# Kernel optimization log

Measured on AMD Instinct MI355X. Metric: run time of the kernel, lower is better.

The kernel has to match this reference:

```python
import jax, jax.numpy as jnp
import numpy as np

EPS_NORM = 1e-12   # F.normalize eps
EPS_PD = 1e-6      # torch pairwise_distance eps
MARGIN = 1.0       # TripletMarginLoss margin


def _l2norm(x, axis):
    n = jnp.sqrt(jnp.sum(x * x, axis=axis, keepdims=True))
    return x / jnp.maximum(n, EPS_NORM)


def setup_inputs() -> dict:
    key = jax.random.key(0)
    k1, k2 = jax.random.split(key)
    query = jax.random.normal(k1, (64, 512, 32, 32), dtype=jnp.float32)
    keys = jax.random.normal(k2, (512, 512), dtype=jnp.float32)
    return {"query": query, "keys": keys}


def reference(query, keys):
    # train=True path of Memory.forward
    B, dims, h, w = query.shape
    m, d = keys.shape
    q = _l2norm(query, axis=1)                       # normalize over channel dim
    q = jnp.transpose(q, (0, 2, 3, 1))               # [B, h, w, d]
    q_flat = q.reshape(B * h * w, d)                 # [N, d]

    score = q_flat @ keys.T                          # [N, m]
    score_query = jax.nn.softmax(score, axis=0)      # softmax over samples per slot
    score_memory = jax.nn.softmax(score, axis=1)     # softmax over slots per sample

    # --- gather loss: MSE(query, keys[argmax slot].detach()) ---
    gather_idx = jnp.argmax(score_memory, axis=1)    # [N]
    nearest = jax.lax.stop_gradient(keys[gather_idx])
    gathering_loss = jnp.mean((q_flat - nearest) ** 2)

    # --- spread loss: triplet(query, 1st-NN slot, 2nd-NN slot) ---
    _, top2 = jax.lax.top_k(score_memory, 2)         # [N, 2]
    pos = jax.lax.stop_gradient(keys[top2[:, 0]])
    neg = jax.lax.stop_gradient(keys[top2[:, 1]])
    d_pos = jnp.linalg.norm(q_flat - pos + EPS_PD, axis=1)
    d_neg = jnp.linalg.norm(q_flat - neg + EPS_PD, axis=1)
    spreading_loss = jnp.mean(jnp.maximum(d_pos - d_neg + MARGIN, 0.0))

    # --- read: attention over memory with detached softmax weights ---
    concat_memory = jax.lax.stop_gradient(score_memory) @ keys      # [N, d]
    updated_query = jnp.concatenate([q_flat, concat_memory], axis=1)
    updated_query = updated_query.reshape(B, h, w, 2 * dims)
    updated_query = jnp.transpose(updated_query, (0, 3, 1, 2))      # [B, 2d, h, w]

    # --- update: argmax-grouped weighted scatter-sum into memory slots ---
    # weight_n = score_query[n, g_n] / max_k score_query[k, g_n]
    col_max = jnp.max(score_query, axis=0)                          # [m]
    wgt = jnp.take_along_axis(score_query, gather_idx[:, None], axis=1)[:, 0]
    wgt = wgt / col_max[gather_idx]                                 # [N]
    query_update = jax.ops.segment_sum(wgt[:, None] * q_flat, gather_idx,
                                       num_segments=m)              # [m, d]
    updated_memory = _l2norm(query_update + keys, axis=1)
    updated_memory = jax.lax.stop_gradient(updated_memory)

    return (updated_query, updated_memory, score_query, score_memory,
            gathering_loss, spreading_loss)
```

## Files before the change

kernel.cpp:

```cpp
#include <hip/hip_runtime.h>
#include <stdint.h>


typedef unsigned int u32;
typedef unsigned long long u64;
typedef unsigned short u16;

typedef float f32x4 __attribute__((ext_vector_type(4)));
typedef short bf16x8 __attribute__((ext_vector_type(8)));

#define DIMS 512

__device__ __forceinline__ u16 f2bf(float x){
  u32 u = __float_as_uint(x);
  return (u16)((u + 0x7FFFu + ((u >> 16) & 1u)) >> 16);
}
__device__ __forceinline__ float bf2f(u16 h){ return __uint_as_float(((u32)h) << 16); }
__device__ __forceinline__ u32 pack2(float a, float b){
  return (u32)f2bf(a) | ((u32)f2bf(b) << 16);
}
__device__ __forceinline__ u32 fkey(float x){
  u32 b = __float_as_uint(x);
  return (b & 0x80000000u) ? ~b : (b | 0x80000000u);
}
__device__ __forceinline__ float fdec(u32 u){
  return (u & 0x80000000u) ? __uint_as_float(u & 0x7FFFFFFFu) : __uint_as_float(~u);
}
__device__ __forceinline__ void gload16(char* lds, const void* g){
  __builtin_amdgcn_global_load_lds(
      (const __attribute__((address_space(1))) u32*)g,
      (__attribute__((address_space(3))) u32*)lds, 16, 0, 0);
}

__global__ __launch_bounds__(512) void k0_prep(const float* __restrict__ keys,
    u16* __restrict__ kb, u16* __restrict__ kt,
    float* __restrict__ kn2, float* __restrict__ ksum,
    u32* __restrict__ colmax_u, float* __restrict__ colsum)
{
  const int j = blockIdx.x, t = threadIdx.x;
  float v = keys[(size_t)j * 512 + t];
  u16 h = f2bf(v);
  kb[(size_t)j * 512 + t] = h;
  kt[(size_t)t * 512 + j] = h;
  float s = v, ss = v * v;
  #pragma unroll
  for (int d = 1; d < 64; d <<= 1){ s += __shfl_xor(s, d); ss += __shfl_xor(ss, d); }
  __shared__ float rs[8], rss[8];
  const int w = t >> 6, lane = t & 63;
  if (lane == 0){ rs[w] = s; rss[w] = ss; }
  __syncthreads();
  if (t == 0){
    float S = 0.f, SS = 0.f;
    for (int i = 0; i < 8; ++i){ S += rs[i]; SS += rss[i]; }
    ksum[j] = S; kn2[j] = SS;
  }
  if (j == 0){ colmax_u[t] = 0u; colsum[t] = 0.f; }
}

__global__ __launch_bounds__(256) void k1_norm(const float* __restrict__ query,
    float* __restrict__ uq, u16* __restrict__ qb, float* __restrict__ sumq)
{
  __shared__ float red[4][64];
  __shared__ float rinvS[64];
  __shared__ float T[64][65];
  const int t = threadIdx.x;
  const int p = t & 63;
  const int cq = t >> 6;
  const int b = blockIdx.y;
  const int p0 = blockIdx.x * 64;
  const float* base = query + (size_t)b * 524288 + p0;

  float v[128];
  float ssq = 0.f;
  #pragma unroll
  for (int k = 0; k < 128; ++k){
    float x = base[(size_t)(cq + 4 * k) * 1024 + p];
    v[k] = x; ssq += x * x;
  }
  red[cq][p] = ssq;
  __syncthreads();
  if (t < 64){
    float tot = red[0][t] + red[1][t] + red[2][t] + red[3][t];
    rinvS[t] = 1.0f / fmaxf(sqrtf(tot), 1e-12f);
  }
  __syncthreads();
  const float rinv = rinvS[p];
  float* uqo = uq + (size_t)b * 1048576 + p0;
  float mysum = 0.f;
  const int r = t >> 2, seg = t & 3;
  for (int cb = 0; cb < 8; ++cb){
    #pragma unroll
    for (int i = 0; i < 16; ++i){
      int c = cb * 64 + cq + i * 4;
      float x = v[cb * 16 + i] * rinv;
      uqo[(size_t)c * 1024 + p] = x;
      T[cq + i * 4][p] = x;
      mysum += x;
    }
    __syncthreads();
    {
      u32 wpk[8];
      #pragma unroll
      for (int k = 0; k < 8; ++k)
        wpk[k] = pack2(T[seg * 16 + 2 * k][r], T[seg * 16 + 2 * k + 1][r]);
      uint4* dst = (uint4*)(qb + ((size_t)(b * 1024 + p0 + r)) * 512 + cb * 64 + seg * 16);
      dst[0] = make_uint4(wpk[0], wpk[1], wpk[2], wpk[3]);
      dst[1] = make_uint4(wpk[4], wpk[5], wpk[6], wpk[7]);
    }
    __syncthreads();
  }
  red[cq][p] = mysum;
  __syncthreads();
  if (t < 64)
    sumq[(size_t)b * 1024 + p0 + t] = red[0][t] + red[1][t] + red[2][t] + red[3][t];
}

__global__ __launch_bounds__(512) void k2f(const u16* __restrict__ Aq,
    const u16* __restrict__ Bk, float* __restrict__ SM,
    u32* __restrict__ colmax_u, float* __restrict__ colsum,
    int* __restrict__ gidx, float* __restrict__ s1v, float* __restrict__ rfac,
    const float* __restrict__ kn2, const float* __restrict__ ksum,
    const float* __restrict__ sumq, float* __restrict__ part)
{
  __shared__ __align__(16) char As[4096];
  __shared__ __align__(16) char Bs[32768];
  __shared__ float rs_m1[8][64], rs_m2[8][64], rs_es[8][64];
  __shared__ int   rs_i1[8][64], rs_i2[8][64];
  __shared__ float rtinv[64];

  const int t = threadIdx.x;
  const int w = t >> 6;
  const int lane = t & 63;
  const int l15 = lane & 15, l4 = lane >> 4;
  const int n0 = blockIdx.x * 64;

  f32x4 acc[4][4];
  #pragma unroll
  for (int a = 0; a < 4; ++a)
    #pragma unroll
    for (int b = 0; b < 4; ++b) acc[a][b] = (f32x4){0.f, 0.f, 0.f, 0.f};

  const int lrow = lane >> 2;
  const int lpos = lane & 3;
  const u16* srcB[4];
  #pragma unroll
  for (int i = 0; i < 4; ++i){
    int r = w * 64 + i * 16 + lrow;
    srcB[i] = Bk + (size_t)r * 512 + ((lpos ^ ((r >> 1) & 3)) * 8);
  }
  const u16* srcA = Aq;
  {
    int r = (w & 3) * 16 + lrow;
    srcA = Aq + (size_t)(n0 + r) * 512 + ((lpos ^ ((r >> 1) & 3)) * 8);
  }
  char* ldsB = Bs + w * 4096;
  char* ldsA = As + (w & 3) * 1024;

  for (int kk = 0; kk < 16; ++kk){
    const int ko = kk * 32;
    __syncthreads();
    #pragma unroll
    for (int i = 0; i < 4; ++i)
      gload16(ldsB + i * 1024, srcB[i] + ko);
    if (w < 4) gload16(ldsA, srcA + ko);
    __syncthreads();
    bf16x8 af[4], bf[4];
    #pragma unroll
    for (int mi = 0; mi < 4; ++mi){
      int rr = mi * 16 + l15;
      af[mi] = *(const bf16x8*)(As + rr * 64 + ((l4 ^ ((rr >> 1) & 3)) * 16));
    }
    #pragma unroll
    for (int nj = 0; nj < 4; ++nj){
      int rb = w * 64 + nj * 16 + l15;
      bf[nj] = *(const bf16x8*)(Bs + rb * 64 + ((l4 ^ ((rb >> 1) & 3)) * 16));
    }
    #pragma unroll
    for (int mi = 0; mi < 4; ++mi)
      #pragma unroll
      for (int nj = 0; nj < 4; ++nj)
        acc[mi][nj] = __builtin_amdgcn_mfma_f32_16x16x32_bf16(af[mi], bf[nj], acc[mi][nj], 0, 0, 0);
  }

  #pragma unroll
  for (int mi = 0; mi < 4; ++mi){
    #pragma unroll
    for (int e = 0; e < 4; ++e){
      const int row = mi * 16 + l4 * 4 + e;
      float m1 = -3e38f, m2 = -3e38f; int i1 = 0x7FFFFFFF, i2 = 0x7FFFFFFF;
      #pragma unroll
      for (int nj = 0; nj < 4; ++nj){
        float val = acc[mi][nj][e];
        int idx = w * 64 + nj * 16 + l15;
        if (val > m1){ m2 = m1; i2 = i1; m1 = val; i1 = idx; }
        else if (val > m2){ m2 = val; i2 = idx; }
      }
      #pragma unroll
      for (int d = 1; d < 16; d <<= 1){
        float o1 = __shfl_xor(m1, d), o2 = __shfl_xor(m2, d);
        int oi1 = __shfl_xor(i1, d), oi2 = __shfl_xor(i2, d);
        if (o1 > m1 || (o1 == m1 && oi1 < i1)){
          if (m1 > o2 || (m1 == o2 && i1 < oi2)){ m2 = m1; i2 = i1; }
          else { m2 = o2; i2 = oi2; }
          m1 = o1; i1 = oi1;
        } else {
          if (o1 > m2 || (o1 == m2 && oi1 < i2)){ m2 = o1; i2 = oi1; }
        }
      }
      if (l15 == 0){
        rs_m1[w][row] = m1; rs_i1[w][row] = i1;
        rs_m2[w][row] = m2; rs_i2[w][row] = i2;
      }
    }
  }
  #pragma unroll
  for (int nj = 0; nj < 4; ++nj){
    float cm = -3e38f;
    #pragma unroll
    for (int mi = 0; mi < 4; ++mi)
      #pragma unroll
      for (int e = 0; e < 4; ++e) cm = fmaxf(cm, acc[mi][nj][e]);
    cm = fmaxf(cm, __shfl_xor(cm, 16));
    cm = fmaxf(cm, __shfl_xor(cm, 32));
    if (l4 == 0) atomicMax(&colmax_u[w * 64 + nj * 16 + l15], fkey(cm));
  }
  #pragma unroll
  for (int mi = 0; mi < 4; ++mi)
    #pragma unroll
    for (int nj = 0; nj < 4; ++nj)
      #pragma unroll
      for (int e = 0; e < 4; ++e) acc[mi][nj][e] = expf(acc[mi][nj][e]);
  #pragma unroll
  for (int mi = 0; mi < 4; ++mi){
    #pragma unroll
    for (int e = 0; e < 4; ++e){
      const int row = mi * 16 + l4 * 4 + e;
      float ps = acc[mi][0][e] + acc[mi][1][e] + acc[mi][2][e] + acc[mi][3][e];
      #pragma unroll
      for (int d = 1; d < 16; d <<= 1) ps += __shfl_xor(ps, d);
      if (l15 == 0) rs_es[w][row] = ps;
    }
  }
  #pragma unroll
  for (int nj = 0; nj < 4; ++nj){
    float cs = 0.f;
    #pragma unroll
    for (int mi = 0; mi < 4; ++mi)
      #pragma unroll
      for (int e = 0; e < 4; ++e) cs += acc[mi][nj][e];
    cs += __shfl_xor(cs, 16);
    cs += __shfl_xor(cs, 32);
    if (l4 == 0) atomicAdd(&colsum[w * 64 + nj * 16 + l15], cs);
  }
  __syncthreads();
  if (t < 64){
    const int row = t, n = n0 + row;
    float m1 = -3e38f, m2 = -3e38f; int i1 = 0x7FFFFFFF, i2 = 0x7FFFFFFF;
    float tot = 0.f;
    #pragma unroll
    for (int w2 = 0; w2 < 8; ++w2){
      float o1 = rs_m1[w2][row], o2 = rs_m2[w2][row];
      int oi1 = rs_i1[w2][row], oi2 = rs_i2[w2][row];
      tot += rs_es[w2][row];
      if (o1 > m1 || (o1 == m1 && oi1 < i1)){
        if (m1 > o2 || (m1 == o2 && i1 < oi2)){ m2 = m1; i2 = i1; }
        else { m2 = o2; i2 = oi2; }
        m1 = o1; i1 = oi1;
      } else {
        if (o1 > m2 || (o1 == m2 && oi1 < i2)){ m2 = o1; i2 = oi1; }
      }
    }
    gidx[n] = i1; s1v[n] = m1; rfac[n] = tot;
    rtinv[row] = 1.0f / tot;
    float sq = sumq[n];
    float gl = 1.0f + kn2[i1] - 2.0f * m1;
    float dp2 = gl + 2e-6f * (sq - ksum[i1]) + 5.12e-10f;
    float dn2 = 1.0f + kn2[i2] - 2.0f * m2 + 2e-6f * (sq - ksum[i2]) + 5.12e-10f;
    float sl = fmaxf(sqrtf(dp2) - sqrtf(dn2) + 1.0f, 0.0f);
    #pragma unroll
    for (int d = 1; d < 64; d <<= 1){ gl += __shfl_xor(gl, d); sl += __shfl_xor(sl, d); }
    if (t == 0){ part[2 * blockIdx.x] = gl; part[2 * blockIdx.x + 1] = sl; }
  }
  __syncthreads();
  #pragma unroll
  for (int mi = 0; mi < 4; ++mi){
    #pragma unroll
    for (int e = 0; e < 4; ++e){
      const int row = mi * 16 + l4 * 4 + e;
      const float ri = rtinv[row];
      float* dst = SM + (size_t)(n0 + row) * 512 + w * 64 + l15;
      #pragma unroll
      for (int nj = 0; nj < 4; ++nj)
        dst[nj * 16] = acc[mi][nj][e] * ri;
    }
  }
}

__global__ __launch_bounds__(256) void k7_update(const int* __restrict__ gidx,
    const float* __restrict__ s1v, const u32* __restrict__ colmax_u,
    const u16* __restrict__ qb, const float* __restrict__ keys, float* __restrict__ um)
{
  const int j = blockIdx.x;
  const int t = threadIdx.x;
  const int lane = t & 63;
  const int w = t >> 6;
  const float cm = fdec(colmax_u[j]);
  float acc[8] = {0.f, 0.f, 0.f, 0.f, 0.f, 0.f, 0.f, 0.f};
  const int b0 = w * 16384, b1 = b0 + 16384;
  for (int base = b0; base < b1; base += 64){
    u64 mask = __ballot(gidx[base + lane] == j);
    while (mask){
      int bpos = (int)__builtin_ctzll(mask);
      mask &= mask - 1;
      int rrow = base + bpos;
      float wgt = expf(s1v[rrow] - cm);
      uint4 rv = *(const uint4*)(qb + (size_t)rrow * 512 + lane * 8);
      u32 a4[4] = {rv.x, rv.y, rv.z, rv.w};
      #pragma unroll
      for (int q = 0; q < 4; ++q){
        acc[2 * q]     += wgt * bf2f((u16)(a4[q] & 0xFFFFu));
        acc[2 * q + 1] += wgt * bf2f((u16)(a4[q] >> 16));
      }
    }
  }
  __shared__ float red[512];
  for (int i = t; i < 512; i += 256) red[i] = 0.f;
  __syncthreads();
  #pragma unroll
  for (int k = 0; k < 8; ++k) atomicAdd(&red[lane * 8 + k], acc[k]);
  __syncthreads();
  float v0 = red[t]       + keys[(size_t)j * 512 + t];
  float v1 = red[t + 256] + keys[(size_t)j * 512 + t + 256];
  float ssq = v0 * v0 + v1 * v1;
  #pragma unroll
  for (int d = 1; d < 64; d <<= 1) ssq += __shfl_xor(ssq, d);
  __shared__ float rr4[4];
  if (lane == 0) rr4[w] = ssq;
  __syncthreads();
  const float rinv = 1.0f / fmaxf(sqrtf(rr4[0] + rr4[1] + rr4[2] + rr4[3]), 1e-12f);
  um[(size_t)j * 512 + t]       = v0 * rinv;
  um[(size_t)j * 512 + t + 256] = v1 * rinv;
}

__global__ __launch_bounds__(512) void k6f(const float* __restrict__ SMf,
    const u16* __restrict__ kt, float* __restrict__ Uq, float* __restrict__ SQ,
    const float* __restrict__ rfac, const float* __restrict__ colsum)
{
  __shared__ __align__(16) char Ks[32768];
  __shared__ __align__(16) char Qs[4096];
  const int t = threadIdx.x;
  const int w = t >> 6;
  const int lane = t & 63;
  const int l15 = lane & 15, l4 = lane >> 4;
  const int n0 = blockIdx.x * 64;

  f32x4 acc[4][4];
  #pragma unroll
  for (int a = 0; a < 4; ++a)
    #pragma unroll
    for (int b = 0; b < 4; ++b) acc[a][b] = (f32x4){0.f, 0.f, 0.f, 0.f};

  const int lrow = lane >> 2;
  const int lpos = lane & 3;
  const u16* srcK[4];
  #pragma unroll
  for (int i = 0; i < 4; ++i){
    int r = w * 64 + i * 16 + lrow;
    srcK[i] = kt + (size_t)r * 512 + ((lpos ^ ((r >> 1) & 3)) * 8);
  }
  char* ldsK = Ks + w * 4096;
  const int rQ = t >> 3;
  const int c4 = (t & 7) * 4;
  const size_t qrow = (size_t)(n0 + rQ) * 512;
  const float rf = rfac[n0 + rQ];
  const int qdst = rQ * 64 + (((c4 >> 3) ^ ((rQ >> 1) & 3)) * 16) + ((c4 & 4) << 1);

  float4 q0 = *(const float4*)(SMf + qrow + c4);

  for (int kk = 0; kk < 16; ++kk){
    const int ko = kk * 32;
    __syncthreads();
    *(u32*)(Qs + qdst)     = pack2(q0.x, q0.y);
    *(u32*)(Qs + qdst + 4) = pack2(q0.z, q0.w);
    #pragma unroll
    for (int i = 0; i < 4; ++i)
      gload16(ldsK + i * 1024, srcK[i] + ko);
    {
      float4 cs = *(const float4*)(colsum + ko + c4);
      float4 sq;
      sq.x = q0.x * rf / cs.x; sq.y = q0.y * rf / cs.y;
      sq.z = q0.z * rf / cs.z; sq.w = q0.w * rf / cs.w;
      *(float4*)(SQ + qrow + ko + c4) = sq;
    }
    __syncthreads();
    if (kk < 15) q0 = *(const float4*)(SMf + qrow + ko + 32 + c4);
    bf16x8 af[4], bf[4];
    #pragma unroll
    for (int mi = 0; mi < 4; ++mi){
      int rr = w * 64 + mi * 16 + l15;
      af[mi] = *(const bf16x8*)(Ks + rr * 64 + ((l4 ^ ((rr >> 1) & 3)) * 16));
    }
    #pragma unroll
    for (int nj = 0; nj < 4; ++nj){
      int rb = nj * 16 + l15;
      bf[nj] = *(const bf16x8*)(Qs + rb * 64 + ((l4 ^ ((rb >> 1) & 3)) * 16));
    }
    #pragma unroll
    for (int mi = 0; mi < 4; ++mi)
      #pragma unroll
      for (int nj = 0; nj < 4; ++nj)
        acc[mi][nj] = __builtin_amdgcn_mfma_f32_16x16x32_bf16(af[mi], bf[nj], acc[mi][nj], 0, 0, 0);
  }

  const int bq = n0 >> 10;
  const int p0 = n0 & 1023;
  #pragma unroll
  for (int mi = 0; mi < 4; ++mi){
    #pragma unroll
    for (int e = 0; e < 4; ++e){
      const int chn = w * 64 + mi * 16 + l4 * 4 + e;
      float* dst = Uq + (size_t)(bq * 1024 + 512 + chn) * 1024 + p0 + l15;
      #pragma unroll
      for (int nj = 0; nj < 4; ++nj)
        dst[nj * 16] = acc[mi][nj][e];
    }
  }
}

__global__ __launch_bounds__(256) void k9_fin(const float* __restrict__ part,
    float* __restrict__ outL)
{
  const int t = threadIdx.x;
  float gs = 0.f, ss = 0.f;
  for (int i = t; i < 1024; i += 256){ gs += part[2 * i]; ss += part[2 * i + 1]; }
  #pragma unroll
  for (int d = 1; d < 64; d <<= 1){ gs += __shfl_xor(gs, d); ss += __shfl_xor(ss, d); }
  __shared__ float rg[4], rs2[4];
  if ((t & 63) == 0){ rg[t >> 6] = gs; rs2[t >> 6] = ss; }
  __syncthreads();
  if (t == 0){
    float G = rg[0] + rg[1] + rg[2] + rg[3];
    float S = rs2[0] + rs2[1] + rs2[2] + rs2[3];
    outL[0] = G / (65536.0f * 512.0f);
    outL[1] = S / 65536.0f;
  }
}

extern "C" void kernel_launch(void* const* d_in, const int* in_sizes, int n_in,
                              void* d_out, int out_size, void* d_ws, size_t ws_size,
                              hipStream_t stream)
{
  int qi = 0, ki = 1;
  if (n_in >= 2 && in_sizes[0] < in_sizes[1]){ qi = 1; ki = 0; }
  const float* query = (const float*)d_in[qi];
  const float* keys  = (const float*)d_in[ki];
  float* out = (float*)d_out;

  const size_t OFF_UQ = 0;
  const size_t OFF_UM = 67108864;
  const size_t OFF_SQ = 67371008;
  const size_t OFF_SM = 100925440;
  const size_t OFF_GL = 134479872;

  u16* qb = (u16*)(out + OFF_SQ);

  char* ws = (char*)d_ws;
  u16*   kb     = (u16*)ws;
  u16*   kt     = (u16*)(ws + 524288);
  float* sumq   = (float*)(ws + 1048576);
  int*   gidx   = (int*)(ws + 1310720);
  float* s1v    = (float*)(ws + 1572864);
  float* rfac   = (float*)(ws + 1835008);
  float* part   = (float*)(ws + 2097152);
  float* kn2    = (float*)(ws + 2105344);
  float* ksum   = (float*)(ws + 2107392);
  u32*   colmax = (u32*)(ws + 2109440);
  float* colsum = (float*)(ws + 2111488);

  k0_prep<<<512, 512, 0, stream>>>(keys, kb, kt, kn2, ksum, colmax, colsum);
  k1_norm<<<dim3(16, 64), 256, 0, stream>>>(query, out + OFF_UQ, qb, sumq);
  k2f<<<1024, 512, 0, stream>>>(qb, kb, out + OFF_SM, colmax, colsum,
                                gidx, s1v, rfac, kn2, ksum, sumq, part);
  k7_update<<<512, 256, 0, stream>>>(gidx, s1v, colmax, qb, keys, out + OFF_UM);
  k6f<<<1024, 512, 0, stream>>>(out + OFF_SM, kt, out + OFF_UQ, out + OFF_SQ,
                                rfac, colsum);
  k9_fin<<<1, 256, 0, stream>>>(part, out + OFF_GL);
}
```

Baseline: 384.5 us.

## Double-buffer LDS tiles in k2f and k6f GEMMs; widen k7_update to 512 threads

The GEMM loops in k2f and k6f now ping-pong between two LDS buffers. Each iteration issues the next k-slice's global-to-LDS loads before running the MFMAs on the current slice, which removes one barrier per iteration and hides load latency. Separately, k7_update runs with 512 threads, so each wave scans half as many samples. The LDS footprint grows to 72KB per block, which may lower occupancy, and the reduction scratch arrays now alias the B buffer region after the loop.

```diff
diff --git a/kernel.cpp b/kernel.cpp
--- a/kernel.cpp
+++ b/kernel.cpp
@@ -122,12 +122,7 @@
     const float* __restrict__ kn2, const float* __restrict__ ksum,
     const float* __restrict__ sumq, float* __restrict__ part)
 {
-  __shared__ __align__(16) char As[4096];
-  __shared__ __align__(16) char Bs[32768];
-  __shared__ float rs_m1[8][64], rs_m2[8][64], rs_es[8][64];
-  __shared__ int   rs_i1[8][64], rs_i2[8][64];
-  __shared__ float rtinv[64];
-
+  __shared__ __align__(16) char smem[73728];
   const int t = threadIdx.x;
   const int w = t >> 6;
   const int lane = t & 63;
@@ -148,22 +143,32 @@
     int r = w * 64 + i * 16 + lrow;
     srcB[i] = Bk + (size_t)r * 512 + ((lpos ^ ((r >> 1) & 3)) * 8);
   }
-  const u16* srcA = Aq;
+  const u16* srcA;
   {
     int r = (w & 3) * 16 + lrow;
     srcA = Aq + (size_t)(n0 + r) * 512 + ((lpos ^ ((r >> 1) & 3)) * 8);
   }
-  char* ldsB = Bs + w * 4096;
-  char* ldsA = As + (w & 3) * 1024;
+
+  {
+    char* ldsB = smem + 8192 + w * 4096;
+    #pragma unroll
+    for (int i = 0; i < 4; ++i) gload16(ldsB + i * 1024, srcB[i]);
+    if (w < 4) gload16(smem + (w & 3) * 1024, srcA);
+  }
+  __syncthreads();
 
   for (int kk = 0; kk < 16; ++kk){
-    const int ko = kk * 32;
-    __syncthreads();
-    #pragma unroll
-    for (int i = 0; i < 4; ++i)
-      gload16(ldsB + i * 1024, srcB[i] + ko);
-    if (w < 4) gload16(ldsA, srcA + ko);
-    __syncthreads();
+    const int cur = kk & 1;
+    if (kk < 15){
+      const int nxt = cur ^ 1;
+      const int ko = (kk + 1) * 32;
+      char* ldsB = smem + 8192 + nxt * 32768 + w * 4096;
+      #pragma unroll
+      for (int i = 0; i < 4; ++i) gload16(ldsB + i * 1024, srcB[i] + ko);
+      if (w < 4) gload16(smem + nxt * 4096 + (w & 3) * 1024, srcA + ko);
+    }
+    const char* As = smem + cur * 4096;
+    const char* Bs = smem + 8192 + cur * 32768;
     bf16x8 af[4], bf[4];
     #pragma unroll
     for (int mi = 0; mi < 4; ++mi){
@@ -180,7 +185,15 @@
       #pragma unroll
       for (int nj = 0; nj < 4; ++nj)
         acc[mi][nj] = __builtin_amdgcn_mfma_f32_16x16x32_bf16(af[mi], bf[nj], acc[mi][nj], 0, 0, 0);
-  }
+    __syncthreads();
+  }
+
+  float* rs_m1 = (float*)(smem + 8192);
+  float* rs_m2 = (float*)(smem + 10240);
+  float* rs_es = (float*)(smem + 12288);
+  int*   rs_i1 = (int*)(smem + 14336);
+  int*   rs_i2 = (int*)(smem + 16384);
+  float* rtinv = (float*)(smem + 18432);
 
   #pragma unroll
   for (int mi = 0; mi < 4; ++mi){
@@ -208,8 +221,8 @@
         }
       }
       if (l15 == 0){
-        rs_m1[w][row] = m1; rs_i1[w][row] = i1;
-        rs_m2[w][row] = m2; rs_i2[w][row] = i2;
+        rs_m1[w * 64 + row] = m1; rs_i1[w * 64 + row] = i1;
+        rs_m2[w * 64 + row] = m2; rs_i2[w * 64 + row] = i2;
       }
     }
   }
@@ -238,7 +251,7 @@
       float ps = acc[mi][0][e] + acc[mi][1][e] + acc[mi][2][e] + acc[mi][3][e];
       #pragma unroll
       for (int d = 1; d < 16; d <<= 1) ps += __shfl_xor(ps, d);
-      if (l15 == 0) rs_es[w][row] = ps;
+      if (l15 == 0) rs_es[w * 64 + row] = ps;
     }
   }
   #pragma unroll
@@ -259,9 +272,9 @@
     float tot = 0.f;
     #pragma unroll
     for (int w2 = 0; w2 < 8; ++w2){
-      float o1 = rs_m1[w2][row], o2 = rs_m2[w2][row];
-      int oi1 = rs_i1[w2][row], oi2 = rs_i2[w2][row];
-      tot += rs_es[w2][row];
+      float o1 = rs_m1[w2 * 64 + row], o2 = rs_m2[w2 * 64 + row];
+      int oi1 = rs_i1[w2 * 64 + row], oi2 = rs_i2[w2 * 64 + row];
+      tot += rs_es[w2 * 64 + row];
       if (o1 > m1 || (o1 == m1 && oi1 < i1)){
         if (m1 > o2 || (m1 == o2 && i1 < oi2)){ m2 = m1; i2 = i1; }
         else { m2 = o2; i2 = oi2; }
@@ -296,7 +309,7 @@
   }
 }
 
-__global__ __launch_bounds__(256) void k7_update(const int* __restrict__ gidx,
+__global__ __launch_bounds__(512) void k7_update(const int* __restrict__ gidx,
     const float* __restrict__ s1v, const u32* __restrict__ colmax_u,
     const u16* __restrict__ qb, const float* __restrict__ keys, float* __restrict__ um)
 {
@@ -306,7 +319,7 @@
   const int w = t >> 6;
   const float cm = fdec(colmax_u[j]);
   float acc[8] = {0.f, 0.f, 0.f, 0.f, 0.f, 0.f, 0.f, 0.f};
-  const int b0 = w * 16384, b1 = b0 + 16384;
+  const int b0 = w * 8192, b1 = b0 + 8192;
   for (int base = b0; base < b1; base += 64){
     u64 mask = __ballot(gidx[base + lane] == j);
     while (mask){
@@ -324,30 +337,28 @@
     }
   }
   __shared__ float red[512];
-  for (int i = t; i < 512; i += 256) red[i] = 0.f;
+  red[t] = 0.f;
   __syncthreads();
   #pragma unroll
   for (int k = 0; k < 8; ++k) atomicAdd(&red[lane * 8 + k], acc[k]);
   __syncthreads();
-  float v0 = red[t]       + keys[(size_t)j * 512 + t];
-  float v1 = red[t + 256] + keys[(size_t)j * 512 + t + 256];
-  float ssq = v0 * v0 + v1 * v1;
+  float v0 = red[t] + keys[(size_t)j * 512 + t];
+  float ssq = v0 * v0;
   #pragma unroll
   for (int d = 1; d < 64; d <<= 1) ssq += __shfl_xor(ssq, d);
-  __shared__ float rr4[4];
-  if (lane == 0) rr4[w] = ssq;
-  __syncthreads();
-  const float rinv = 1.0f / fmaxf(sqrtf(rr4[0] + rr4[1] + rr4[2] + rr4[3]), 1e-12f);
-  um[(size_t)j * 512 + t]       = v0 * rinv;
-  um[(size_t)j * 512 + t + 256] = v1 * rinv;
+  __shared__ float rr8[8];
+  if (lane == 0) rr8[w] = ssq;
+  __syncthreads();
+  float tot = rr8[0] + rr8[1] + rr8[2] + rr8[3] + rr8[4] + rr8[5] + rr8[6] + rr8[7];
+  const float rinv = 1.0f / fmaxf(sqrtf(tot), 1e-12f);
+  um[(size_t)j * 512 + t] = v0 * rinv;
 }
 
 __global__ __launch_bounds__(512) void k6f(const float* __restrict__ SMf,
     const u16* __restrict__ kt, float* __restrict__ Uq, float* __restrict__ SQ,
     const float* __restrict__ rfac, const float* __restrict__ colsum)
 {
-  __shared__ __align__(16) char Ks[32768];
-  __shared__ __align__(16) char Qs[4096];
+  __shared__ __align__(16) char smem[73728];
   const int t = threadIdx.x;
   const int w = t >> 6;
   const int lane = t & 63;
@@ -368,32 +379,49 @@
     int r = w * 64 + i * 16 + lrow;
     srcK[i] = kt + (size_t)r * 512 + ((lpos ^ ((r >> 1) & 3)) * 8);
   }
-  char* ldsK = Ks + w * 4096;
   const int rQ = t >> 3;
   const int c4 = (t & 7) * 4;
   const size_t qrow = (size_t)(n0 + rQ) * 512;
   const float rf = rfac[n0 + rQ];
   const int qdst = rQ * 64 + (((c4 >> 3) ^ ((rQ >> 1) & 3)) * 16) + ((c4 & 4) << 1);
 
-  float4 q0 = *(const float4*)(SMf + qrow + c4);
+  float4 qcur = *(const float4*)(SMf + qrow + c4);
+  {
+    char* Qs0 = smem + 65536;
+    *(u32*)(Qs0 + qdst)     = pack2(qcur.x, qcur.y);
+    *(u32*)(Qs0 + qdst + 4) = pack2(qcur.z, qcur.w);
+    float4 cs = *(const float4*)(colsum + c4);
+    float4 sq;
+    sq.x = qcur.x * rf / cs.x; sq.y = qcur.y * rf / cs.y;
+    sq.z = qcur.z * rf / cs.z; sq.w = qcur.w * rf / cs.w;
+    *(float4*)(SQ + qrow + c4) = sq;
+    char* ldsK = smem + w * 4096;
+    #pragma unroll
+    for (int i = 0; i < 4; ++i) gload16(ldsK + i * 1024, srcK[i]);
+  }
+  float4 qnext = *(const float4*)(SMf + qrow + 32 + c4);
+  __syncthreads();
 
   for (int kk = 0; kk < 16; ++kk){
-    const int ko = kk * 32;
-    __syncthreads();
-    *(u32*)(Qs + qdst)     = pack2(q0.x, q0.y);
-    *(u32*)(Qs + qdst + 4) = pack2(q0.z, q0.w);
-    #pragma unroll
-    for (int i = 0; i < 4; ++i)
-      gload16(ldsK + i * 1024, srcK[i] + ko);
-    {
+    const int cur = kk & 1;
+    if (kk < 15){
+      const int nxt = cur ^ 1;
+      const int ko = (kk + 1) * 32;
+      char* ldsK = smem + nxt * 32768 + w * 4096;
+      #pragma unroll
+      for (int i = 0; i < 4; ++i) gload16(ldsK + i * 1024, srcK[i] + ko);
+      char* QsN = smem + 65536 + nxt * 4096;
+      *(u32*)(QsN + qdst)     = pack2(qnext.x, qnext.y);
+      *(u32*)(QsN + qdst + 4) = pack2(qnext.z, qnext.w);
       float4 cs = *(const float4*)(colsum + ko + c4);
       float4 sq;
-      sq.x = q0.x * rf / cs.x; sq.y = q0.y * rf / cs.y;
-      sq.z = q0.z * rf / cs.z; sq.w = q0.w * rf / cs.w;
+      sq.x = qnext.x * rf / cs.x; sq.y = qnext.y * rf / cs.y;
+      sq.z = qnext.z * rf / cs.z; sq.w = qnext.w * rf / cs.w;
       *(float4*)(SQ + qrow + ko + c4) = sq;
-    }
-    __syncthreads();
-    if (kk < 15) q0 = *(const float4*)(SMf + qrow + ko + 32 + c4);
+      if (kk < 14) qnext = *(const float4*)(SMf + qrow + ko + 32 + c4);
+    }
+    const char* Ks = smem + cur * 32768;
+    const char* Qs = smem + 65536 + cur * 4096;
     bf16x8 af[4], bf[4];
     #pragma unroll
     for (int mi = 0; mi < 4; ++mi){
@@ -410,6 +438,7 @@
       #pragma unroll
       for (int nj = 0; nj < 4; ++nj)
         acc[mi][nj] = __builtin_amdgcn_mfma_f32_16x16x32_bf16(af[mi], bf[nj], acc[mi][nj], 0, 0, 0);
+    __syncthreads();
   }
 
   const int bq = n0 >> 10;
@@ -481,7 +510,7 @@
   k1_norm<<<dim3(16, 64), 256, 0, stream>>>(query, out + OFF_UQ, qb, sumq);
   k2f<<<1024, 512, 0, stream>>>(qb, kb, out + OFF_SM, colmax, colsum,
                                 gidx, s1v, rfac, kn2, ksum, sumq, part);
-  k7_update<<<512, 256, 0, stream>>>(gidx, s1v, colmax, qb, keys, out + OFF_UM);
+  k7_update<<<512, 512, 0, stream>>>(gidx, s1v, colmax, qb, keys, out + OFF_UM);
   k6f<<<1024, 512, 0, stream>>>(out + OFF_SM, kt, out + OFF_UQ, out + OFF_SQ,
                                 rfac, colsum);
   k9_fin<<<1, 256, 0, stream>>>(part, out + OFF_GL);
```

Measured after the change: 375.0 us (median of 2 runs). 1.03x faster.

## Replace LDS staging in GEMM kernels with direct register double-buffered loads

Applied to the files above, without the earlier changes.

Both MFMA GEMM kernels (k2f score and k6f read) drop their LDS tiles, barriers and global_load_lds staging. Each wave now loads its bf16x8 fragments straight from global memory into registers, double-buffered across k-steps, and raises wave priority around the MFMA bursts. In k6f the fp32 softmax rows are converted to bf16 in registers, and wave 0 alone writes score_query using precomputed reciprocals. k7_update moves to 512 threads per block so each wave scans half as many rows. The trade is that every wave re-fetches shared A/B data from global or L2 memory instead of sharing one LDS copy, in exchange for removing the syncthreads stalls, and register pressure goes up.

```diff
diff --git a/kernel.cpp b/kernel.cpp
--- a/kernel.cpp
+++ b/kernel.cpp
@@ -25,11 +25,6 @@
 }
 __device__ __forceinline__ float fdec(u32 u){
   return (u & 0x80000000u) ? __uint_as_float(u & 0x7FFFFFFFu) : __uint_as_float(~u);
-}
-__device__ __forceinline__ void gload16(char* lds, const void* g){
-  __builtin_amdgcn_global_load_lds(
-      (const __attribute__((address_space(1))) u32*)g,
-      (__attribute__((address_space(3))) u32*)lds, 16, 0, 0);
 }
 
 __global__ __launch_bounds__(512) void k0_prep(const float* __restrict__ keys,
@@ -122,8 +117,6 @@
     const float* __restrict__ kn2, const float* __restrict__ ksum,
     const float* __restrict__ sumq, float* __restrict__ part)
 {
-  __shared__ __align__(16) char As[4096];
-  __shared__ __align__(16) char Bs[32768];
   __shared__ float rs_m1[8][64], rs_m2[8][64], rs_es[8][64];
   __shared__ int   rs_i1[8][64], rs_i2[8][64];
   __shared__ float rtinv[64];
@@ -140,46 +133,48 @@
     #pragma unroll
     for (int b = 0; b < 4; ++b) acc[a][b] = (f32x4){0.f, 0.f, 0.f, 0.f};
 
-  const int lrow = lane >> 2;
-  const int lpos = lane & 3;
-  const u16* srcB[4];
-  #pragma unroll
-  for (int i = 0; i < 4; ++i){
-    int r = w * 64 + i * 16 + lrow;
-    srcB[i] = Bk + (size_t)r * 512 + ((lpos ^ ((r >> 1) & 3)) * 8);
-  }
-  const u16* srcA = Aq;
-  {
-    int r = (w & 3) * 16 + lrow;
-    srcA = Aq + (size_t)(n0 + r) * 512 + ((lpos ^ ((r >> 1) & 3)) * 8);
-  }
-  char* ldsB = Bs + w * 4096;
-  char* ldsA = As + (w & 3) * 1024;
-
-  for (int kk = 0; kk < 16; ++kk){
-    const int ko = kk * 32;
-    __syncthreads();
-    #pragma unroll
-    for (int i = 0; i < 4; ++i)
-      gload16(ldsB + i * 1024, srcB[i] + ko);
-    if (w < 4) gload16(ldsA, srcA + ko);
-    __syncthreads();
-    bf16x8 af[4], bf[4];
-    #pragma unroll
-    for (int mi = 0; mi < 4; ++mi){
-      int rr = mi * 16 + l15;
-      af[mi] = *(const bf16x8*)(As + rr * 64 + ((l4 ^ ((rr >> 1) & 3)) * 16));
-    }
-    #pragma unroll
-    for (int nj = 0; nj < 4; ++nj){
-      int rb = w * 64 + nj * 16 + l15;
-      bf[nj] = *(const bf16x8*)(Bs + rb * 64 + ((l4 ^ ((rb >> 1) & 3)) * 16));
-    }
+  const u16* ap[4];
+  const u16* bp[4];
+  #pragma unroll
+  for (int mi = 0; mi < 4; ++mi)
+    ap[mi] = Aq + (size_t)(n0 + mi * 16 + l15) * 512 + l4 * 8;
+  #pragma unroll
+  for (int nj = 0; nj < 4; ++nj)
+    bp[nj] = Bk + (size_t)(w * 64 + nj * 16 + l15) * 512 + l4 * 8;
+
+  bf16x8 a0[4], b0[4], a1[4], b1[4];
+  #pragma unroll
+  for (int mi = 0; mi < 4; ++mi) a0[mi] = *(const bf16x8*)(ap[mi]);
+  #pragma unroll
+  for (int nj = 0; nj < 4; ++nj) b0[nj] = *(const bf16x8*)(bp[nj]);
+
+  for (int kk = 0; kk < 16; kk += 2){
+    const int ko1 = (kk + 1) * 32;
+    #pragma unroll
+    for (int mi = 0; mi < 4; ++mi) a1[mi] = *(const bf16x8*)(ap[mi] + ko1);
+    #pragma unroll
+    for (int nj = 0; nj < 4; ++nj) b1[nj] = *(const bf16x8*)(bp[nj] + ko1);
+    __builtin_amdgcn_s_setprio(1);
     #pragma unroll
     for (int mi = 0; mi < 4; ++mi)
       #pragma unroll
       for (int nj = 0; nj < 4; ++nj)
-        acc[mi][nj] = __builtin_amdgcn_mfma_f32_16x16x32_bf16(af[mi], bf[nj], acc[mi][nj], 0, 0, 0);
+        acc[mi][nj] = __builtin_amdgcn_mfma_f32_16x16x32_bf16(a0[mi], b0[nj], acc[mi][nj], 0, 0, 0);
+    __builtin_amdgcn_s_setprio(0);
+    if (kk + 2 < 16){
+      const int ko2 = (kk + 2) * 32;
+      #pragma unroll
+      for (int mi = 0; mi < 4; ++mi) a0[mi] = *(const bf16x8*)(ap[mi] + ko2);
+      #pragma unroll
+      for (int nj = 0; nj < 4; ++nj) b0[nj] = *(const bf16x8*)(bp[nj] + ko2);
+    }
+    __builtin_amdgcn_s_setprio(1);
+    #pragma unroll
+    for (int mi = 0; mi < 4; ++mi)
+      #pragma unroll
+      for (int nj = 0; nj < 4; ++nj)
+        acc[mi][nj] = __builtin_amdgcn_mfma_f32_16x16x32_bf16(a1[mi], b1[nj], acc[mi][nj], 0, 0, 0);
+    __builtin_amdgcn_s_setprio(0);
   }
 
   #pragma unroll
@@ -296,7 +291,7 @@
   }
 }
 
-__global__ __launch_bounds__(256) void k7_update(const int* __restrict__ gidx,
+__global__ __launch_bounds__(512) void k7_update(const int* __restrict__ gidx,
     const float* __restrict__ s1v, const u32* __restrict__ colmax_u,
     const u16* __restrict__ qb, const float* __restrict__ keys, float* __restrict__ um)
 {
@@ -306,7 +301,7 @@
   const int w = t >> 6;
   const float cm = fdec(colmax_u[j]);
   float acc[8] = {0.f, 0.f, 0.f, 0.f, 0.f, 0.f, 0.f, 0.f};
-  const int b0 = w * 16384, b1 = b0 + 16384;
+  const int b0 = w * 8192, b1 = b0 + 8192;
   for (int base = b0; base < b1; base += 64){
     u64 mask = __ballot(gidx[base + lane] == j);
     while (mask){
@@ -324,30 +319,27 @@
     }
   }
   __shared__ float red[512];
-  for (int i = t; i < 512; i += 256) red[i] = 0.f;
+  red[t] = 0.f;
   __syncthreads();
   #pragma unroll
   for (int k = 0; k < 8; ++k) atomicAdd(&red[lane * 8 + k], acc[k]);
   __syncthreads();
-  float v0 = red[t]       + keys[(size_t)j * 512 + t];
-  float v1 = red[t + 256] + keys[(size_t)j * 512 + t + 256];
-  float ssq = v0 * v0 + v1 * v1;
+  float v0 = red[t] + keys[(size_t)j * 512 + t];
+  float ssq = v0 * v0;
   #pragma unroll
   for (int d = 1; d < 64; d <<= 1) ssq += __shfl_xor(ssq, d);
-  __shared__ float rr4[4];
-  if (lane == 0) rr4[w] = ssq;
-  __syncthreads();
-  const float rinv = 1.0f / fmaxf(sqrtf(rr4[0] + rr4[1] + rr4[2] + rr4[3]), 1e-12f);
-  um[(size_t)j * 512 + t]       = v0 * rinv;
-  um[(size_t)j * 512 + t + 256] = v1 * rinv;
+  __shared__ float rr8[8];
+  if (lane == 0) rr8[w] = ssq;
+  __syncthreads();
+  float tot = rr8[0] + rr8[1] + rr8[2] + rr8[3] + rr8[4] + rr8[5] + rr8[6] + rr8[7];
+  const float rinv = 1.0f / fmaxf(sqrtf(tot), 1e-12f);
+  um[(size_t)j * 512 + t] = v0 * rinv;
 }
 
 __global__ __launch_bounds__(512) void k6f(const float* __restrict__ SMf,
     const u16* __restrict__ kt, float* __restrict__ Uq, float* __restrict__ SQ,
     const float* __restrict__ rfac, const float* __restrict__ colsum)
 {
-  __shared__ __align__(16) char Ks[32768];
-  __shared__ __align__(16) char Qs[4096];
   const int t = threadIdx.x;
   const int w = t >> 6;
   const int lane = t & 63;
@@ -360,56 +352,122 @@
     #pragma unroll
     for (int b = 0; b < 4; ++b) acc[a][b] = (f32x4){0.f, 0.f, 0.f, 0.f};
 
-  const int lrow = lane >> 2;
-  const int lpos = lane & 3;
-  const u16* srcK[4];
-  #pragma unroll
-  for (int i = 0; i < 4; ++i){
-    int r = w * 64 + i * 16 + lrow;
-    srcK[i] = kt + (size_t)r * 512 + ((lpos ^ ((r >> 1) & 3)) * 8);
-  }
-  char* ldsK = Ks + w * 4096;
-  const int rQ = t >> 3;
-  const int c4 = (t & 7) * 4;
-  const size_t qrow = (size_t)(n0 + rQ) * 512;
-  const float rf = rfac[n0 + rQ];
-  const int qdst = rQ * 64 + (((c4 >> 3) ^ ((rQ >> 1) & 3)) * 16) + ((c4 & 4) << 1);
-
-  float4 q0 = *(const float4*)(SMf + qrow + c4);
-
-  for (int kk = 0; kk < 16; ++kk){
-    const int ko = kk * 32;
-    __syncthreads();
-    *(u32*)(Qs + qdst)     = pack2(q0.x, q0.y);
-    *(u32*)(Qs + qdst + 4) = pack2(q0.z, q0.w);
-    #pragma unroll
-    for (int i = 0; i < 4; ++i)
-      gload16(ldsK + i * 1024, srcK[i] + ko);
+  const u16* ap[4];
+  const float* bpf[4];
+  #pragma unroll
+  for (int mi = 0; mi < 4; ++mi)
+    ap[mi] = kt + (size_t)(w * 64 + mi * 16 + l15) * 512 + l4 * 8;
+  #pragma unroll
+  for (int nj = 0; nj < 4; ++nj)
+    bpf[nj] = SMf + (size_t)(n0 + nj * 16 + l15) * 512 + l4 * 8;
+
+  float rf4[4];
+  #pragma unroll
+  for (int nj = 0; nj < 4; ++nj) rf4[nj] = rfac[n0 + nj * 16 + l15];
+
+  bf16x8 a0[4], a1[4];
+  float4 pA[4][2], pB[4][2];
+  #pragma unroll
+  for (int mi = 0; mi < 4; ++mi) a0[mi] = *(const bf16x8*)(ap[mi]);
+  #pragma unroll
+  for (int nj = 0; nj < 4; ++nj){
+    pA[nj][0] = *(const float4*)(bpf[nj]);
+    pA[nj][1] = *(const float4*)(bpf[nj] + 4);
+  }
+
+  for (int kk = 0; kk < 16; kk += 2){
+    const int ko1 = (kk + 1) * 32;
+    #pragma unroll
+    for (int mi = 0; mi < 4; ++mi) a1[mi] = *(const bf16x8*)(ap[mi] + ko1);
+    #pragma unroll
+    for (int nj = 0; nj < 4; ++nj){
+      pB[nj][0] = *(const float4*)(bpf[nj] + ko1);
+      pB[nj][1] = *(const float4*)(bpf[nj] + ko1 + 4);
+    }
     {
-      float4 cs = *(const float4*)(colsum + ko + c4);
-      float4 sq;
-      sq.x = q0.x * rf / cs.x; sq.y = q0.y * rf / cs.y;
-      sq.z = q0.z * rf / cs.z; sq.w = q0.w * rf / cs.w;
-      *(float4*)(SQ + qrow + ko + c4) = sq;
-    }
-    __syncthreads();
-    if (kk < 15) q0 = *(const float4*)(SMf + qrow + ko + 32 + c4);
-    bf16x8 af[4], bf[4];
-    #pragma unroll
-    for (int mi = 0; mi < 4; ++mi){
-      int rr = w * 64 + mi * 16 + l15;
-      af[mi] = *(const bf16x8*)(Ks + rr * 64 + ((l4 ^ ((rr >> 1) & 3)) * 16));
-    }
-    #pragma unroll
-    for (int nj = 0; nj < 4; ++nj){
-      int rb = nj * 16 + l15;
-      bf[nj] = *(const bf16x8*)(Qs + rb * 64 + ((l4 ^ ((rb >> 1) & 3)) * 16));
-    }
-    #pragma unroll
-    for (int mi = 0; mi < 4; ++mi)
-      #pragma unroll
-      for (int nj = 0; nj < 4; ++nj)
-        acc[mi][nj] = __builtin_amdgcn_mfma_f32_16x16x32_bf16(af[mi], bf[nj], acc[mi][nj], 0, 0, 0);
+      bf16x8 bb[4];
+      u32* bw;
+      #pragma unroll
+      for (int nj = 0; nj < 4; ++nj){
+        u32 w0 = pack2(pA[nj][0].x, pA[nj][0].y);
+        u32 w1 = pack2(pA[nj][0].z, pA[nj][0].w);
+        u32 w2 = pack2(pA[nj][1].x, pA[nj][1].y);
+        u32 w3 = pack2(pA[nj][1].z, pA[nj][1].w);
+        bw = (u32*)&bb[nj];
+        bw[0] = w0; bw[1] = w1; bw[2] = w2; bw[3] = w3;
+      }
+      if (w == 0){
+        const int cbase = kk * 32 + l4 * 8;
+        float4 cs0 = *(const float4*)(colsum + cbase);
+        float4 cs1 = *(const float4*)(colsum + cbase + 4);
+        float4 ci0 = {1.f / cs0.x, 1.f / cs0.y, 1.f / cs0.z, 1.f / cs0.w};
+        float4 ci1 = {1.f / cs1.x, 1.f / cs1.y, 1.f / cs1.z, 1.f / cs1.w};
+        #pragma unroll
+        for (int nj = 0; nj < 4; ++nj){
+          float* d = SQ + (size_t)(n0 + nj * 16 + l15) * 512 + cbase;
+          float4 s0 = {pA[nj][0].x * rf4[nj] * ci0.x, pA[nj][0].y * rf4[nj] * ci0.y,
+                       pA[nj][0].z * rf4[nj] * ci0.z, pA[nj][0].w * rf4[nj] * ci0.w};
+          float4 s1 = {pA[nj][1].x * rf4[nj] * ci1.x, pA[nj][1].y * rf4[nj] * ci1.y,
+                       pA[nj][1].z * rf4[nj] * ci1.z, pA[nj][1].w * rf4[nj] * ci1.w};
+          *(float4*)(d) = s0;
+          *(float4*)(d + 4) = s1;
+        }
+      }
+      __builtin_amdgcn_s_setprio(1);
+      #pragma unroll
+      for (int mi = 0; mi < 4; ++mi)
+        #pragma unroll
+        for (int nj = 0; nj < 4; ++nj)
+          acc[mi][nj] = __builtin_amdgcn_mfma_f32_16x16x32_bf16(a0[mi], bb[nj], acc[mi][nj], 0, 0, 0);
+      __builtin_amdgcn_s_setprio(0);
+    }
+    if (kk + 2 < 16){
+      const int ko2 = (kk + 2) * 32;
+      #pragma unroll
+      for (int mi = 0; mi < 4; ++mi) a0[mi] = *(const bf16x8*)(ap[mi] + ko2);
+      #pragma unroll
+      for (int nj = 0; nj < 4; ++nj){
+        pA[nj][0] = *(const float4*)(bpf[nj] + ko2);
+        pA[nj][1] = *(const float4*)(bpf[nj] + ko2 + 4);
+      }
+    }
+    {
+      bf16x8 bb[4];
+      u32* bw;
+      #pragma unroll
+      for (int nj = 0; nj < 4; ++nj){
+        u32 w0 = pack2(pB[nj][0].x, pB[nj][0].y);
+        u32 w1 = pack2(pB[nj][0].z, pB[nj][0].w);
+        u32 w2 = pack2(pB[nj][1].x, pB[nj][1].y);
+        u32 w3 = pack2(pB[nj][1].z, pB[nj][1].w);
+        bw = (u32*)&bb[nj];
+        bw[0] = w0; bw[1] = w1; bw[2] = w2; bw[3] = w3;
+      }
+      if (w == 0){
+        const int cbase = (kk + 1) * 32 + l4 * 8;
+        float4 cs0 = *(const float4*)(colsum + cbase);
+        float4 cs1 = *(const float4*)(colsum + cbase + 4);
+        float4 ci0 = {1.f / cs0.x, 1.f / cs0.y, 1.f / cs0.z, 1.f / cs0.w};
+        float4 ci1 = {1.f / cs1.x, 1.f / cs1.y, 1.f / cs1.z, 1.f / cs1.w};
+        #pragma unroll
+        for (int nj = 0; nj < 4; ++nj){
+          float* d = SQ + (size_t)(n0 + nj * 16 + l15) * 512 + cbase;
+          float4 s0 = {pB[nj][0].x * rf4[nj] * ci0.x, pB[nj][0].y * rf4[nj] * ci0.y,
+                       pB[nj][0].z * rf4[nj] * ci0.z, pB[nj][0].w * rf4[nj] * ci0.w};
+          float4 s1 = {pB[nj][1].x * rf4[nj] * ci1.x, pB[nj][1].y * rf4[nj] * ci1.y,
+                       pB[nj][1].z * rf4[nj] * ci1.z, pB[nj][1].w * rf4[nj] * ci1.w};
+          *(float4*)(d) = s0;
+          *(float4*)(d + 4) = s1;
+        }
+      }
+      __builtin_amdgcn_s_setprio(1);
+      #pragma unroll
+      for (int mi = 0; mi < 4; ++mi)
+        #pragma unroll
+        for (int nj = 0; nj < 4; ++nj)
+          acc[mi][nj] = __builtin_amdgcn_mfma_f32_16x16x32_bf16(a1[mi], bb[nj], acc[mi][nj], 0, 0, 0);
+      __builtin_amdgcn_s_setprio(0);
+    }
   }
 
   const int bq = n0 >> 10;
@@ -481,7 +539,7 @@
   k1_norm<<<dim3(16, 64), 256, 0, stream>>>(query, out + OFF_UQ, qb, sumq);
   k2f<<<1024, 512, 0, stream>>>(qb, kb, out + OFF_SM, colmax, colsum,
                                 gidx, s1v, rfac, kn2, ksum, sumq, part);
-  k7_update<<<512, 256, 0, stream>>>(gidx, s1v, colmax, qb, keys, out + OFF_UM);
+  k7_update<<<512, 512, 0, stream>>>(gidx, s1v, colmax, qb, keys, out + OFF_UM);
   k6f<<<1024, 512, 0, stream>>>(out + OFF_SM, kt, out + OFF_UQ, out + OFF_SQ,
                                 rfac, colsum);
   k9_fin<<<1, 256, 0, stream>>>(part, out + OFF_GL);
```

Result: slower. 591.1 us (+53.7%).
